# Optimization experiments

Hardware: AMD Instinct MI355X
Metric: run time of the kernel (lower is better)

## Reference

```python
import jax, jax.numpy as jnp
import numpy as np

VOCAB, EMB, HID, FF, NCLS = 1000, 32, 32, 16, 7
T, B = 512, 512


def setup_inputs() -> dict:
    key = jax.random.key(0)
    ks = jax.random.split(key, 10)
    s = 1.0 / np.sqrt(HID)
    return {
        "x": jax.random.randint(ks[0], (T, B), 0, VOCAB, dtype=jnp.int64)
        if jax.config.jax_enable_x64 else jax.random.randint(ks[0], (T, B), 0, VOCAB, dtype=jnp.int32),
        "emb": jax.random.normal(ks[1], (VOCAB, EMB), dtype=jnp.float32),
        "W_ih": jax.random.uniform(ks[2], (4 * HID, EMB), minval=-s, maxval=s, dtype=jnp.float32),
        "W_hh": jax.random.uniform(ks[3], (4 * HID, HID), minval=-s, maxval=s, dtype=jnp.float32),
        "b_ih": jax.random.uniform(ks[4], (4 * HID,), minval=-s, maxval=s, dtype=jnp.float32),
        "b_hh": jax.random.uniform(ks[5], (4 * HID,), minval=-s, maxval=s, dtype=jnp.float32),
        "W1": jax.random.uniform(ks[6], (FF, HID), minval=-s, maxval=s, dtype=jnp.float32),
        "b1": jax.random.uniform(ks[7], (FF,), minval=-s, maxval=s, dtype=jnp.float32),
        "W2": jax.random.uniform(ks[8], (NCLS, FF), minval=-s, maxval=s, dtype=jnp.float32),
        "b2": jax.random.uniform(ks[9], (NCLS,), minval=-s, maxval=s, dtype=jnp.float32),
    }


def _lstm(xg, W_hh):
    # xg: (T, B, 4H) precomputed input-to-gate projections (incl. both biases)
    Bn = xg.shape[1]
    h0 = jnp.zeros((Bn, HID), xg.dtype)
    c0 = jnp.zeros((Bn, HID), xg.dtype)

    def step(carry, xg_t):
        h, c = carry
        g = xg_t + h @ W_hh.T  # (B, 4H)
        i, f, gg, o = jnp.split(g, 4, axis=-1)  # PyTorch gate order i,f,g,o
        i = jax.nn.sigmoid(i)
        f = jax.nn.sigmoid(f)
        gg = jnp.tanh(gg)
        o = jax.nn.sigmoid(o)
        c = f * c + i * gg
        h = o * jnp.tanh(c)
        return (h, c), h

    _, hs = jax.lax.scan(step, (h0, c0), xg)
    return hs  # (T, B, H)


def reference(x, emb, W_ih, W_hh, b_ih, b_hh, W1, b1, W2, b2):
    e = emb[x]  # (T, B, EMB) embedding lookup
    xg = jnp.einsum('tbe,ge->tbg', e, W_ih) + b_ih + b_hh  # (T, B, 4H)
    hs = _lstm(xg, W_hh)  # (T, B, H)
    z = jax.nn.relu(jnp.einsum('tbh,fh->tbf', hs, W1) + b1)  # (T, B, FF)
    logits = jnp.einsum('tbf,cf->tbc', z, W2) + b2  # (T, B, NCLS)
    # torch F.softmax with dim=None on a 3D tensor softmaxes over dim 0
    return jax.nn.softmax(logits, axis=0)
```

## Files before the change

kernel.cpp:

```cpp
#include <hip/hip_runtime.h>
#include <math.h>

#define TT    512
#define BB    512
#define HID   32
#define EMB   32
#define FFD   16
#define NCLS  7
#define VOCABN 1000

__device__ __forceinline__ float rl(float v, int k) {
    return __int_as_float(__builtin_amdgcn_readlane(__float_as_int(v), k));
}
__device__ __forceinline__ float fast_rcp(float x) {
#if defined(__has_builtin)
#if __has_builtin(__builtin_amdgcn_rcpf)
    return __builtin_amdgcn_rcpf(x);
#else
    return 1.0f / x;
#endif
#else
    return 1.0f / x;
#endif
}
__device__ __forceinline__ float sigf(float x) { return fast_rcp(1.0f + __expf(-x)); }
__device__ __forceinline__ float tanh_fast(float x) { return 2.0f * sigf(2.0f * x) - 1.0f; }

__device__ __forceinline__ float xhalf_swap(float v) {
#if defined(__has_builtin)
#if __has_builtin(__builtin_amdgcn_permlane32_swap)
    const unsigned u = __float_as_uint(v);
    auto r = __builtin_amdgcn_permlane32_swap(u, u, false, false);
    return __uint_as_float((r[0] ^ r[1]) ^ u);
#else
    return __shfl_xor(v, 32);
#endif
#else
    return __shfl_xor(v, 32);
#endif
}

__global__ __launch_bounds__(64) void build_xg(
    const float* __restrict__ emb, const float* __restrict__ W_ih,
    const float* __restrict__ b_ih, const float* __restrict__ b_hh,
    float2* __restrict__ tab)
{
    const int v = blockIdx.x;
    const int j = threadIdx.x;
    const float* e  = emb + v * EMB;
    const float* w0 = W_ih + j * EMB;
    const float* w1 = W_ih + (j + 64) * EMB;
    float a0 = b_ih[j]      + b_hh[j];
    float a1 = b_ih[j + 64] + b_hh[j + 64];
    #pragma unroll
    for (int k = 0; k < EMB; ++k) {
        const float ek = e[k];
        a0 = fmaf(w0[k], ek, a0);
        a1 = fmaf(w1[k], ek, a1);
    }
    tab[v * 64 + j] = make_float2(a0, a1);
}

__global__ __launch_bounds__(64, 1) void lstm_rec(
    const int* __restrict__ x, const float2* __restrict__ tab,
    const float* __restrict__ W_hh, float* __restrict__ hsout)
{
    const int b  = blockIdx.x;
    const int j  = threadIdx.x;
    const int m  = j & 31;
    const bool lo = j < 32;

    __shared__ float sh[8 * HID];

    float whhA[HID], whhB[HID];
    #pragma unroll
    for (int k = 0; k < HID; k += 4) {
        float4 a;
        a = *(const float4*)(W_hh + j * HID + k);        whhA[k]=a.x; whhA[k+1]=a.y; whhA[k+2]=a.z; whhA[k+3]=a.w;
        a = *(const float4*)(W_hh + (j + 64) * HID + k); whhB[k]=a.x; whhB[k+1]=a.y; whhB[k+2]=a.z; whhB[k+3]=a.w;
    }
    #define PIN16(A, base) \
        asm volatile("" : "+v"((A)[(base)+0]), "+v"((A)[(base)+1]), "+v"((A)[(base)+2]), "+v"((A)[(base)+3]), \
                          "+v"((A)[(base)+4]), "+v"((A)[(base)+5]), "+v"((A)[(base)+6]), "+v"((A)[(base)+7]), \
                          "+v"((A)[(base)+8]), "+v"((A)[(base)+9]), "+v"((A)[(base)+10]), "+v"((A)[(base)+11]), \
                          "+v"((A)[(base)+12]), "+v"((A)[(base)+13]), "+v"((A)[(base)+14]), "+v"((A)[(base)+15]))
    PIN16(whhA, 0); PIN16(whhA, 16);
    PIN16(whhB, 0); PIN16(whhB, 16);
    #undef PIN16

    float h = 0.f, c = 0.f;
    float* hrow0 = hsout + (size_t)b * TT * HID;

    int xiB[8];
    float2 cxg[8];
    {
        int xi0[8];
        #pragma unroll
        for (int u = 0; u < 8; ++u) xi0[u] = x[u * BB + b];
        #pragma unroll
        for (int u = 0; u < 8; ++u) xiB[u] = x[(8 + u) * BB + b];
        #pragma unroll
        for (int u = 0; u < 8; ++u) cxg[u] = tab[(size_t)xi0[u] * 64 + j];
    }

    for (int t8 = 0; t8 < TT / 8; ++t8) {
        float2 nxg[8];
        #pragma unroll
        for (int u = 0; u < 8; ++u) nxg[u] = tab[(size_t)xiB[u] * 64 + j];
        int xiN[8];
        const int nb2 = (t8 + 2 < TT / 8) ? (t8 + 2) * 8 : 0;
        #pragma unroll
        for (int u = 0; u < 8; ++u) xiN[u] = x[(nb2 + u) * BB + b];

        #pragma unroll
        for (int u = 0; u < 8; ++u) {
            float hs[HID];
            #pragma unroll
            for (int k = 0; k < HID; ++k) hs[k] = rl(h, k);

            float p0 = cxg[u].x, p1 = 0.f, p2 = 0.f, p3 = 0.f;
            float q0 = cxg[u].y, q1 = 0.f, q2 = 0.f, q3 = 0.f;
            #pragma unroll
            for (int k = 0; k < HID; k += 4) {
                p0 = fmaf(whhA[k],   hs[k],   p0);
                p1 = fmaf(whhA[k+1], hs[k+1], p1);
                p2 = fmaf(whhA[k+2], hs[k+2], p2);
                p3 = fmaf(whhA[k+3], hs[k+3], p3);
                q0 = fmaf(whhB[k],   hs[k],   q0);
                q1 = fmaf(whhB[k+1], hs[k+1], q1);
                q2 = fmaf(whhB[k+2], hs[k+2], q2);
                q3 = fmaf(whhB[k+3], hs[k+3], q3);
            }
            const float accA = (p0 + p1) + (p2 + p3);
            const float accB = (q0 + q1) + (q2 + q3);

            const float actA = sigf(accA);
            const float sB   = lo ? 2.0f * accB : accB;
            const float sgB  = sigf(sB);
            const float actB = lo ? 2.0f * sgB - 1.0f : sgB;
            const float oA = xhalf_swap(actA);
            const float oB = xhalf_swap(actB);
            const float gi = lo ? actA : oA;
            const float gf = lo ? oA   : actA;
            const float gg = lo ? actB : oB;
            const float go = lo ? oB   : actB;
            c = fmaf(gf, c, gi * gg);
            h = go * tanh_fast(c);

            if (lo) sh[u * HID + m] = h;
        }
        const float4 v = *(const float4*)(sh + j * 4);
        *(float4*)(hrow0 + t8 * 8 * HID + j * 4) = v;

        #pragma unroll
        for (int u = 0; u < 8; ++u) { cxg[u] = nxg[u]; xiB[u] = xiN[u]; }
    }
}

__global__ __launch_bounds__(256) void ff_softmax(
    const float* __restrict__ hs,
    const float* __restrict__ W1, const float* __restrict__ b1,
    const float* __restrict__ W2, const float* __restrict__ b2,
    float* __restrict__ out)
{
    const int b    = blockIdx.x;
    const int tid  = threadIdx.x;
    const int lane = tid & 63, wv = tid >> 6;
    const int t0   = tid * 2;

    __shared__ float redM[4][NCLS];
    __shared__ float redS[4][NCLS];

    float4 hv[16];
    const float4* hb = (const float4*)(hs + ((size_t)b * TT + t0) * HID);
    #pragma unroll
    for (int q = 0; q < 16; ++q) hv[q] = hb[q];

    float lg[2][NCLS];
    #pragma unroll
    for (int r = 0; r < 2; ++r) {
        const float* hr = (const float*)(hv + 8 * r);
        float z[FFD];
        #pragma unroll
        for (int f = 0; f < FFD; ++f) {
            float a = b1[f];
            #pragma unroll
            for (int k = 0; k < HID; ++k) a = fmaf(W1[f * HID + k], hr[k], a);
            z[f] = fmaxf(a, 0.f);
        }
        #pragma unroll
        for (int cc = 0; cc < NCLS; ++cc) {
            float a = b2[cc];
            #pragma unroll
            for (int f = 0; f < FFD; ++f) a = fmaf(W2[cc * FFD + f], z[f], a);
            lg[r][cc] = a;
        }
    }

    float M[NCLS], S[NCLS];
    #pragma unroll
    for (int cc = 0; cc < NCLS; ++cc) {
        float mm = fmaxf(lg[0][cc], lg[1][cc]);
        #pragma unroll
        for (int off = 32; off; off >>= 1) mm = fmaxf(mm, __shfl_xor(mm, off));
        if (lane == 0) redM[wv][cc] = mm;
    }
    __syncthreads();
    #pragma unroll
    for (int cc = 0; cc < NCLS; ++cc)
        M[cc] = fmaxf(fmaxf(redM[0][cc], redM[1][cc]), fmaxf(redM[2][cc], redM[3][cc]));

    #pragma unroll
    for (int cc = 0; cc < NCLS; ++cc) {
        float ss = __expf(lg[0][cc] - M[cc]) + __expf(lg[1][cc] - M[cc]);
        #pragma unroll
        for (int off = 32; off; off >>= 1) ss += __shfl_xor(ss, off);
        if (lane == 0) redS[wv][cc] = ss;
    }
    __syncthreads();
    #pragma unroll
    for (int cc = 0; cc < NCLS; ++cc)
        S[cc] = (redS[0][cc] + redS[1][cc]) + (redS[2][cc] + redS[3][cc]);

    #pragma unroll
    for (int r = 0; r < 2; ++r) {
        float* o = out + ((size_t)(t0 + r) * BB + b) * NCLS;
        #pragma unroll
        for (int cc = 0; cc < NCLS; ++cc)
            o[cc] = __expf(lg[r][cc] - M[cc]) * fast_rcp(S[cc]);
    }
}

template <bool TAB>
__global__ __launch_bounds__(64) void lstm_all(
    const int* __restrict__ x, const float* __restrict__ emb,
    const float* __restrict__ W_ih, const float* __restrict__ W_hh,
    const float* __restrict__ b_ih, const float* __restrict__ b_hh,
    const float* __restrict__ W1, const float* __restrict__ b1,
    const float* __restrict__ W2, const float* __restrict__ b2,
    const float2* __restrict__ tab, float* __restrict__ out)
{
    const int b  = blockIdx.x;
    const int j  = threadIdx.x;
    const int m  = j & 31;
    const bool lo = j < 32;
    const int rA = j, rB = j + 64;

    float whhA[HID], whhB[HID];
    #pragma unroll
    for (int k = 0; k < HID; k += 4) {
        float4 a;
        a = *(const float4*)(W_hh + rA * HID + k); whhA[k]=a.x; whhA[k+1]=a.y; whhA[k+2]=a.z; whhA[k+3]=a.w;
        a = *(const float4*)(W_hh + rB * HID + k); whhB[k]=a.x; whhB[k+1]=a.y; whhB[k+2]=a.z; whhB[k+3]=a.w;
    }
    float wihA[HID], wihB[HID];
    float biasA = 0.f, biasB = 0.f;
    if constexpr (!TAB) {
        #pragma unroll
        for (int k = 0; k < HID; k += 4) {
            float4 a;
            a = *(const float4*)(W_ih + rA * HID + k); wihA[k]=a.x; wihA[k+1]=a.y; wihA[k+2]=a.z; wihA[k+3]=a.w;
            a = *(const float4*)(W_ih + rB * HID + k); wihB[k]=a.x; wihB[k+1]=a.y; wihB[k+2]=a.z; wihB[k+3]=a.w;
        }
        biasA = b_ih[rA] + b_hh[rA];
        biasB = b_ih[rB] + b_hh[rB];
    }
    const int f16 = j & 15;
    float w1r[HID];
    #pragma unroll
    for (int k = 0; k < HID; ++k) w1r[k] = W1[f16 * HID + k];
    const int cls = j & 7;
    const int c7  = (cls < NCLS) ? cls : 0;
    float w2r[FFD];
    #pragma unroll
    for (int f = 0; f < FFD; ++f) w2r[f] = W2[c7 * FFD + f];
    const float b1v = b1[f16];
    const float b2v = b2[c7];

    float h = 0.f, c = 0.f;
    float mrun = -3.0e38f, srun = 0.f;

    auto gates = [&](float accA, float accB) {
        const float actA = sigf(accA);
        const float sB   = lo ? 2.0f * accB : accB;
        const float sgB  = sigf(sB);
        const float actB = lo ? 2.0f * sgB - 1.0f : sgB;
        const float oA = __shfl_xor(actA, 32);
        const float oB = __shfl_xor(actB, 32);
        const float gi = lo ? actA : oA;
        const float gf = lo ? oA   : actA;
        const float gg = lo ? actB : oB;
        const float go = lo ? oB   : actB;
        c = fmaf(gf, c, gi * gg);
        h = go * tanh_fast(c);
    };

    auto ff_head = [&](int t_out, const float* hsv) {
        float z0 = b1v, z1 = 0.f;
        #pragma unroll
        for (int k = 0; k < HID; k += 2) {
            z0 = fmaf(w1r[k],     hsv[k],     z0);
            z1 = fmaf(w1r[k + 1], hsv[k + 1], z1);
        }
        const float z = fmaxf(z0 + z1, 0.0f);
        float lgv = b2v;
        #pragma unroll
        for (int f = 0; f < FFD; ++f) lgv = fmaf(w2r[f], rl(z, f), lgv);
        const float mn = fmaxf(mrun, lgv);
        srun = fmaf(srun, __expf(mrun - mn), __expf(lgv - mn));
        mrun = mn;
        if (j < NCLS) out[(t_out * BB + b) * NCLS + j] = lgv;
    };

    int xvn1 = x[1 * BB + b];
    int xvn2 = x[2 * BB + b];
    float2 xg = make_float2(0.f, 0.f);
    float eA = 0.f;
    if constexpr (TAB) xg = tab[(size_t)x[b] * 64 + j];
    else               eA = emb[x[b] * EMB + m];

    if constexpr (TAB) {
        gates(xg.x, xg.y);
    } else {
        float es[EMB];
        #pragma unroll
        for (int k = 0; k < EMB; ++k) es[k] = rl(eA, k);
        float p0 = biasA, p1 = 0.f, q0 = biasB, q1 = 0.f;
        #pragma unroll
        for (int k = 0; k < EMB; k += 2) {
            p0 = fmaf(wihA[k],   es[k],   p0); p1 = fmaf(wihA[k+1], es[k+1], p1);
            q0 = fmaf(wihB[k],   es[k],   q0); q1 = fmaf(wihB[k+1], es[k+1], q1);
        }
        gates(p0 + p1, q0 + q1);
    }
    if constexpr (TAB) xg = tab[(size_t)xvn1 * 64 + j];
    else               eA = emb[xvn1 * EMB + m];
    xvn1 = xvn2;
    xvn2 = x[3 * BB + b];

    for (int t = 1; t < TT; ++t) {
        float2 xg_n = make_float2(0.f, 0.f);
        float  e_n  = 0.f;
        if (t + 1 < TT) {
            if constexpr (TAB) xg_n = tab[(size_t)xvn1 * 64 + j];
            else               e_n  = emb[xvn1 * EMB + m];
        }
        const int xv_n3 = (t + 3 < TT) ? x[(t + 3) * BB + b] : 0;

        float hsv[HID];
        #pragma unroll
        for (int k = 0; k < HID; ++k) hsv[k] = rl(h, k);

        ff_head(t - 1, hsv);

        float p0, p1 = 0.f, q0, q1 = 0.f;
        if constexpr (TAB) { p0 = xg.x; q0 = xg.y; }
        else               { p0 = biasA; q0 = biasB; }
        if constexpr (!TAB) {
            float es[EMB];
            #pragma unroll
            for (int k = 0; k < EMB; ++k) es[k] = rl(eA, k);
            #pragma unroll
            for (int k = 0; k < EMB; k += 2) {
                p0 = fmaf(wihA[k],   es[k],   p0); p1 = fmaf(wihA[k+1], es[k+1], p1);
                q0 = fmaf(wihB[k],   es[k],   q0); q1 = fmaf(wihB[k+1], es[k+1], q1);
            }
        }
        #pragma unroll
        for (int k = 0; k < HID; k += 2) {
            p0 = fmaf(whhA[k],   hsv[k],   p0); p1 = fmaf(whhA[k+1], hsv[k+1], p1);
            q0 = fmaf(whhB[k],   hsv[k],   q0); q1 = fmaf(whhB[k+1], hsv[k+1], q1);
        }
        gates(p0 + p1, q0 + q1);

        xg = xg_n; eA = e_n; xvn1 = xvn2; xvn2 = xv_n3;
    }

    {
        float hsv[HID];
        #pragma unroll
        for (int k = 0; k < HID; ++k) hsv[k] = rl(h, k);
        ff_head(TT - 1, hsv);
    }

    #pragma unroll 1
    for (int cc = 0; cc < NCLS; ++cc) {
        const float mc = rl(mrun, cc);
        const float sc = rl(srun, cc);
        const float ic = 1.0f / sc;
        #pragma unroll
        for (int i = 0; i < TT / 64; ++i) {
            const int t = j + 64 * i;
            const int a = (t * BB + b) * NCLS + cc;
            out[a] = __expf(out[a] - mc) * ic;
        }
    }
}

extern "C" void kernel_launch(void* const* d_in, const int* in_sizes, int n_in,
                              void* d_out, int out_size, void* d_ws, size_t ws_size,
                              hipStream_t stream) {
    const int*   x   = (const int*)  d_in[0];
    const float* emb = (const float*)d_in[1];
    const float* Wih = (const float*)d_in[2];
    const float* Whh = (const float*)d_in[3];
    const float* bih = (const float*)d_in[4];
    const float* bhh = (const float*)d_in[5];
    const float* W1  = (const float*)d_in[6];
    const float* b1  = (const float*)d_in[7];
    const float* W2  = (const float*)d_in[8];
    const float* b2  = (const float*)d_in[9];
    float* out = (float*)d_out;

    const size_t tab_bytes = (size_t)VOCABN * 128 * sizeof(float);
    const size_t hs_off    = 524288;
    const size_t hs_bytes  = (size_t)BB * TT * HID * sizeof(float);
    if (ws_size >= hs_off + hs_bytes) {
        float2* tab = (float2*)d_ws;
        float*  hs  = (float*)((char*)d_ws + hs_off);
        build_xg<<<VOCABN, 64, 0, stream>>>(emb, Wih, bih, bhh, tab);
        lstm_rec<<<BB, 64, 0, stream>>>(x, tab, Whh, hs);
        ff_softmax<<<BB, 256, 0, stream>>>(hs, W1, b1, W2, b2, out);
    } else if (ws_size >= tab_bytes) {
        float2* tab = (float2*)d_ws;
        build_xg<<<VOCABN, 64, 0, stream>>>(emb, Wih, bih, bhh, tab);
        lstm_all<true><<<BB, 64, 0, stream>>>(x, emb, Wih, Whh, bih, bhh,
                                              W1, b1, W2, b2, tab, out);
    } else {
        lstm_all<false><<<BB, 64, 0, stream>>>(x, emb, Wih, Whh, bih, bhh,
                                               W1, b1, W2, b2, nullptr, out);
    }
}
```

Before: 257.8 us.

## Prescale gate weights by -log2e, broadcast h via LDS, use packed FMA

The input-projection table and the recurrent weights are pre-multiplied by -log2(e), or -2·log2(e) for the tanh gate, so each activation becomes exp2 plus a reciprocal with no per-step scaling. The 32 readlane broadcasts of h per step are replaced by eight 16-byte LDS reads from the previous step's slot in the shared buffer. The matvec now uses packed 2-wide FMAs on v2f vectors. This is meant to shorten the serial per-step dependency chain, at the cost of an LDS round trip on that chain and a small change in rounding.

Result: faster. 240.1 us (-6.9%).

```diff
diff --git a/kernel.cpp b/kernel.cpp
--- a/kernel.cpp
+++ b/kernel.cpp
@@ -9,6 +9,12 @@
 #define NCLS  7
 #define VOCABN 1000
 
+typedef float v2f __attribute__((ext_vector_type(2)));
+typedef float v4f __attribute__((ext_vector_type(4)));
+
+#define NLOG2E  (-1.4426950408889634f)
+#define N2LOG2E (-2.8853900817779268f)
+
 __device__ __forceinline__ float rl(float v, int k) {
     return __int_as_float(__builtin_amdgcn_readlane(__float_as_int(v), k));
 }
@@ -25,6 +31,18 @@
 }
 __device__ __forceinline__ float sigf(float x) { return fast_rcp(1.0f + __expf(-x)); }
 __device__ __forceinline__ float tanh_fast(float x) { return 2.0f * sigf(2.0f * x) - 1.0f; }
+
+__device__ __forceinline__ v2f fma2(v2f a, v2f b, v2f c) {
+#if defined(__has_builtin)
+#if __has_builtin(__builtin_elementwise_fma)
+    return __builtin_elementwise_fma(a, b, c);
+#else
+    v2f r; r.x = fmaf(a.x, b.x, c.x); r.y = fmaf(a.y, b.y, c.y); return r;
+#endif
+#else
+    v2f r; r.x = fmaf(a.x, b.x, c.x); r.y = fmaf(a.y, b.y, c.y); return r;
+#endif
+}
 
 __device__ __forceinline__ float xhalf_swap(float v) {
 #if defined(__has_builtin)
@@ -43,7 +61,7 @@
 __global__ __launch_bounds__(64) void build_xg(
     const float* __restrict__ emb, const float* __restrict__ W_ih,
     const float* __restrict__ b_ih, const float* __restrict__ b_hh,
-    float2* __restrict__ tab)
+    float2* __restrict__ tab, int scaled)
 {
     const int v = blockIdx.x;
     const int j = threadIdx.x;
@@ -58,10 +76,14 @@
         a0 = fmaf(w0[k], ek, a0);
         a1 = fmaf(w1[k], ek, a1);
     }
-    tab[v * 64 + j] = make_float2(a0, a1);
-}
-
-__global__ __launch_bounds__(64, 1) void lstm_rec(
+    float s0 = 1.0f, s1 = 1.0f;
+    if (scaled) { s0 = NLOG2E; s1 = (j < 32) ? N2LOG2E : NLOG2E; }
+    tab[v * 64 + j] = make_float2(a0 * s0, a1 * s1);
+}
+
+__global__ __launch_bounds__(64)
+__attribute__((amdgpu_waves_per_eu(1, 1)))
+void lstm_rec(
     const int* __restrict__ x, const float2* __restrict__ tab,
     const float* __restrict__ W_hh, float* __restrict__ hsout)
 {
@@ -70,26 +92,38 @@
     const int m  = j & 31;
     const bool lo = j < 32;
 
-    __shared__ float sh[8 * HID];
-
-    float whhA[HID], whhB[HID];
-    #pragma unroll
-    for (int k = 0; k < HID; k += 4) {
-        float4 a;
-        a = *(const float4*)(W_hh + j * HID + k);        whhA[k]=a.x; whhA[k+1]=a.y; whhA[k+2]=a.z; whhA[k+3]=a.w;
-        a = *(const float4*)(W_hh + (j + 64) * HID + k); whhB[k]=a.x; whhB[k+1]=a.y; whhB[k+2]=a.z; whhB[k+3]=a.w;
-    }
-    #define PIN16(A, base) \
-        asm volatile("" : "+v"((A)[(base)+0]), "+v"((A)[(base)+1]), "+v"((A)[(base)+2]), "+v"((A)[(base)+3]), \
-                          "+v"((A)[(base)+4]), "+v"((A)[(base)+5]), "+v"((A)[(base)+6]), "+v"((A)[(base)+7]), \
-                          "+v"((A)[(base)+8]), "+v"((A)[(base)+9]), "+v"((A)[(base)+10]), "+v"((A)[(base)+11]), \
-                          "+v"((A)[(base)+12]), "+v"((A)[(base)+13]), "+v"((A)[(base)+14]), "+v"((A)[(base)+15]))
-    PIN16(whhA, 0); PIN16(whhA, 16);
-    PIN16(whhB, 0); PIN16(whhB, 16);
-    #undef PIN16
+    __shared__ __align__(16) float sh[8 * HID];
+
+    const float fA = NLOG2E;
+    const float fB = lo ? N2LOG2E : NLOG2E;
+    const v2f sA2 = {fA, fA};
+    const v2f sB2 = {fB, fB};
+    const v4f* WA = (const v4f*)(W_hh + j * HID);
+    const v4f* WB = (const v4f*)(W_hh + (j + 64) * HID);
+    v4f t;
+    v2f wpa0,wpa1,wpa2,wpa3,wpa4,wpa5,wpa6,wpa7,wpa8,wpa9,wpa10,wpa11,wpa12,wpa13,wpa14,wpa15;
+    v2f wpb0,wpb1,wpb2,wpb3,wpb4,wpb5,wpb6,wpb7,wpb8,wpb9,wpb10,wpb11,wpb12,wpb13,wpb14,wpb15;
+    t = WA[0]; wpa0  = t.lo * sA2; wpa1  = t.hi * sA2;
+    t = WA[1]; wpa2  = t.lo * sA2; wpa3  = t.hi * sA2;
+    t = WA[2]; wpa4  = t.lo * sA2; wpa5  = t.hi * sA2;
+    t = WA[3]; wpa6  = t.lo * sA2; wpa7  = t.hi * sA2;
+    t = WA[4]; wpa8  = t.lo * sA2; wpa9  = t.hi * sA2;
+    t = WA[5]; wpa10 = t.lo * sA2; wpa11 = t.hi * sA2;
+    t = WA[6]; wpa12 = t.lo * sA2; wpa13 = t.hi * sA2;
+    t = WA[7]; wpa14 = t.lo * sA2; wpa15 = t.hi * sA2;
+    t = WB[0]; wpb0  = t.lo * sB2; wpb1  = t.hi * sB2;
+    t = WB[1]; wpb2  = t.lo * sB2; wpb3  = t.hi * sB2;
+    t = WB[2]; wpb4  = t.lo * sB2; wpb5  = t.hi * sB2;
+    t = WB[3]; wpb6  = t.lo * sB2; wpb7  = t.hi * sB2;
+    t = WB[4]; wpb8  = t.lo * sB2; wpb9  = t.hi * sB2;
+    t = WB[5]; wpb10 = t.lo * sB2; wpb11 = t.hi * sB2;
+    t = WB[6]; wpb12 = t.lo * sB2; wpb13 = t.hi * sB2;
+    t = WB[7]; wpb14 = t.lo * sB2; wpb15 = t.hi * sB2;
 
     float h = 0.f, c = 0.f;
     float* hrow0 = hsout + (size_t)b * TT * HID;
+
+    if (lo) sh[7 * HID + m] = 0.0f;
 
     int xiB[8];
     float2 cxg[8];
@@ -114,30 +148,42 @@
 
         #pragma unroll
         for (int u = 0; u < 8; ++u) {
-            float hs[HID];
-            #pragma unroll
-            for (int k = 0; k < HID; ++k) hs[k] = rl(h, k);
-
-            float p0 = cxg[u].x, p1 = 0.f, p2 = 0.f, p3 = 0.f;
-            float q0 = cxg[u].y, q1 = 0.f, q2 = 0.f, q3 = 0.f;
-            #pragma unroll
-            for (int k = 0; k < HID; k += 4) {
-                p0 = fmaf(whhA[k],   hs[k],   p0);
-                p1 = fmaf(whhA[k+1], hs[k+1], p1);
-                p2 = fmaf(whhA[k+2], hs[k+2], p2);
-                p3 = fmaf(whhA[k+3], hs[k+3], p3);
-                q0 = fmaf(whhB[k],   hs[k],   q0);
-                q1 = fmaf(whhB[k+1], hs[k+1], q1);
-                q2 = fmaf(whhB[k+2], hs[k+2], q2);
-                q3 = fmaf(whhB[k+3], hs[k+3], q3);
-            }
-            const float accA = (p0 + p1) + (p2 + p3);
-            const float accB = (q0 + q1) + (q2 + q3);
-
-            const float actA = sigf(accA);
-            const float sB   = lo ? 2.0f * accB : accB;
-            const float sgB  = sigf(sB);
-            const float actB = lo ? 2.0f * sgB - 1.0f : sgB;
+            const float* hb = sh + ((u + 7) & 7) * HID;
+            const v4f h0 = *(const v4f*)(hb + 0);
+            const v4f h1 = *(const v4f*)(hb + 4);
+            const v4f h2 = *(const v4f*)(hb + 8);
+            const v4f h3 = *(const v4f*)(hb + 12);
+            const v4f h4 = *(const v4f*)(hb + 16);
+            const v4f h5 = *(const v4f*)(hb + 20);
+            const v4f h6 = *(const v4f*)(hb + 24);
+            const v4f h7 = *(const v4f*)(hb + 28);
+
+            v2f aP0 = {cxg[u].x, 0.f}, aP1 = {0.f, 0.f};
+            v2f aQ0 = {cxg[u].y, 0.f}, aQ1 = {0.f, 0.f};
+            aP0 = fma2(wpa0,  h0.lo, aP0);  aP1 = fma2(wpa1,  h0.hi, aP1);
+            aQ0 = fma2(wpb0,  h0.lo, aQ0);  aQ1 = fma2(wpb1,  h0.hi, aQ1);
+            aP0 = fma2(wpa2,  h1.lo, aP0);  aP1 = fma2(wpa3,  h1.hi, aP1);
+            aQ0 = fma2(wpb2,  h1.lo, aQ0);  aQ1 = fma2(wpb3,  h1.hi, aQ1);
+            aP0 = fma2(wpa4,  h2.lo, aP0);  aP1 = fma2(wpa5,  h2.hi, aP1);
+            aQ0 = fma2(wpb4,  h2.lo, aQ0);  aQ1 = fma2(wpb5,  h2.hi, aQ1);
+            aP0 = fma2(wpa6,  h3.lo, aP0);  aP1 = fma2(wpa7,  h3.hi, aP1);
+            aQ0 = fma2(wpb6,  h3.lo, aQ0);  aQ1 = fma2(wpb7,  h3.hi, aQ1);
+            aP0 = fma2(wpa8,  h4.lo, aP0);  aP1 = fma2(wpa9,  h4.hi, aP1);
+            aQ0 = fma2(wpb8,  h4.lo, aQ0);  aQ1 = fma2(wpb9,  h4.hi, aQ1);
+            aP0 = fma2(wpa10, h5.lo, aP0);  aP1 = fma2(wpa11, h5.hi, aP1);
+            aQ0 = fma2(wpb10, h5.lo, aQ0);  aQ1 = fma2(wpb11, h5.hi, aQ1);
+            aP0 = fma2(wpa12, h6.lo, aP0);  aP1 = fma2(wpa13, h6.hi, aP1);
+            aQ0 = fma2(wpb12, h6.lo, aQ0);  aQ1 = fma2(wpb13, h6.hi, aQ1);
+            aP0 = fma2(wpa14, h7.lo, aP0);  aP1 = fma2(wpa15, h7.hi, aP1);
+            aQ0 = fma2(wpb14, h7.lo, aQ0);  aQ1 = fma2(wpb15, h7.hi, aQ1);
+            const v2f aP = aP0 + aP1;
+            const v2f aQ = aQ0 + aQ1;
+            const float accA = aP.x + aP.y;
+            const float accB = aQ.x + aQ.y;
+
+            const float actA = fast_rcp(1.0f + __builtin_exp2f(accA));
+            const float sgB  = fast_rcp(1.0f + __builtin_exp2f(accB));
+            const float actB = lo ? fmaf(2.0f, sgB, -1.0f) : sgB;
             const float oA = xhalf_swap(actA);
             const float oB = xhalf_swap(actB);
             const float gi = lo ? actA : oA;
@@ -145,7 +191,9 @@
             const float gg = lo ? actB : oB;
             const float go = lo ? oB   : actB;
             c = fmaf(gf, c, gi * gg);
-            h = go * tanh_fast(c);
+            const float tc = fmaf(2.0f,
+                fast_rcp(1.0f + __builtin_exp2f(c * N2LOG2E)), -1.0f);
+            h = go * tc;
 
             if (lo) sh[u * HID + m] = h;
         }
@@ -418,12 +466,12 @@
     if (ws_size >= hs_off + hs_bytes) {
         float2* tab = (float2*)d_ws;
         float*  hs  = (float*)((char*)d_ws + hs_off);
-        build_xg<<<VOCABN, 64, 0, stream>>>(emb, Wih, bih, bhh, tab);
+        build_xg<<<VOCABN, 64, 0, stream>>>(emb, Wih, bih, bhh, tab, 1);
         lstm_rec<<<BB, 64, 0, stream>>>(x, tab, Whh, hs);
         ff_softmax<<<BB, 256, 0, stream>>>(hs, W1, b1, W2, b2, out);
     } else if (ws_size >= tab_bytes) {
         float2* tab = (float2*)d_ws;
-        build_xg<<<VOCABN, 64, 0, stream>>>(emb, Wih, bih, bhh, tab);
+        build_xg<<<VOCABN, 64, 0, stream>>>(emb, Wih, bih, bhh, tab, 0);
         lstm_all<true><<<BB, 64, 0, stream>>>(x, emb, Wih, Whh, bih, bhh,
                                               W1, b1, W2, b2, tab, out);
     } else {
```
